# Optimization experiments

Hardware: AMD Instinct MI355X
Metric: run time of the kernel (lower is better)

Reference implementation:

```python
import jax, jax.numpy as jnp
import numpy as np

N = 20000      # nodes
E = 320000     # edges (before self-loops)
F_IN = 50      # PPI num_features
C1 = 256       # per-head channels, conv1/conv2
H1 = 4         # heads, conv1/conv2
C3 = 121       # PPI num_classes, conv3 per-head channels
H3 = 6         # heads, conv3 (concat=False -> mean)


def gat_conv(x, src, dst, W, a_src, a_dst, b, heads, ch, concat, n):
    """PyG-style GATConv with self-loops already included in (src, dst).
    Messages flow src -> dst; softmax is over incoming edges of each dst node."""
    h = (x @ W).reshape(n, heads, ch)                      # [N, H, C]
    es = jnp.sum(h * a_src, axis=-1)                       # [N, H]
    ed = jnp.sum(h * a_dst, axis=-1)                       # [N, H]
    e = jax.nn.leaky_relu(es[src] + ed[dst], 0.2)          # [E', H]
    m = jax.ops.segment_max(e, dst, num_segments=n)        # stable softmax per dst
    e = jnp.exp(e - m[dst])
    denom = jax.ops.segment_sum(e, dst, num_segments=n)
    alpha = e / jnp.maximum(denom[dst], 1e-16)             # [E', H]
    out = jax.ops.segment_sum(alpha[:, :, None] * h[src], dst, num_segments=n)  # [N, H, C]
    out = out.reshape(n, heads * ch) if concat else out.mean(axis=1)
    return out + b


def setup_inputs() -> dict:
    key = jax.random.key(0)
    ks = jax.random.split(key, 16)

    def p(k, shape, fan_in):
        return (jax.random.normal(k, shape, jnp.float32) / np.float32(np.sqrt(fan_in)))

    x = jax.random.normal(ks[0], (N, F_IN), jnp.float32)
    edge_index = jax.random.randint(ks[1], (2, E), 0, N, dtype=jnp.int64)
    D1 = H1 * C1  # 1024
    return dict(
        x=x, edge_index=edge_index,
        W1=p(ks[2], (F_IN, D1), F_IN), a1s=p(ks[3], (H1, C1), C1), a1d=p(ks[4], (H1, C1), C1), b1=jnp.zeros((D1,), jnp.float32),
        Wl1=p(ks[5], (F_IN, D1), F_IN), bl1=jnp.zeros((D1,), jnp.float32),
        W2=p(ks[6], (D1, D1), D1), a2s=p(ks[7], (H1, C1), C1), a2d=p(ks[8], (H1, C1), C1), b2=jnp.zeros((D1,), jnp.float32),
        Wl2=p(ks[9], (D1, D1), D1), bl2=jnp.zeros((D1,), jnp.float32),
        W3=p(ks[10], (D1, H3 * C3), D1), a3s=p(ks[11], (H3, C3), C3), a3d=p(ks[12], (H3, C3), C3), b3=jnp.zeros((C3,), jnp.float32),
        Wl3=p(ks[13], (D1, C3), D1), bl3=jnp.zeros((C3,), jnp.float32),
    )


def reference(x, edge_index, W1, a1s, a1d, b1, Wl1, bl1, W2, a2s, a2d, b2, Wl2, bl2, W3, a3s, a3d, b3, Wl3, bl3):
    n = x.shape[0]
    loop = jnp.arange(n, dtype=edge_index.dtype)           # PyG GATConv adds self-loops
    src = jnp.concatenate([edge_index[0], loop])
    dst = jnp.concatenate([edge_index[1], loop])
    x1 = jax.nn.elu(gat_conv(x, src, dst, W1, a1s, a1d, b1, H1, C1, True, n) + x @ Wl1 + bl1)
    x2 = jax.nn.elu(gat_conv(x1, src, dst, W2, a2s, a2d, b2, H1, C1, True, n) + x1 @ Wl2 + bl2)
    out = gat_conv(x2, src, dst, W3, a3s, a3d, b3, H3, C3, False, n) + x2 @ Wl3 + bl3
    return out
```

## Files before the change

kernel.cpp:

```cpp
#include <hip/hip_runtime.h>
#include <hip/hip_bf16.h>
#include <math.h>

typedef __bf16 bf16;
typedef __attribute__((ext_vector_type(4))) __bf16 bf16x4;
typedef __attribute__((ext_vector_type(8))) __bf16 bf16x8;
typedef __attribute__((ext_vector_type(4))) float f32x4;

#define N_NODES 20000
#define N_EDGES 320000
#define E2 (N_EDGES + N_NODES)
#define F_IN 50
#define D1 1024
#define NP12 2048
#define NP3 896
#define SG 2048
#define KA 320

#define PO_A1S 0
#define PO_A1D 1024
#define PO_B1  2048
#define PO_BL1 3072
#define PO_A2S 4096
#define PO_A2D 5120
#define PO_B2  6144
#define PO_BL2 7168
#define PO_A3S 8192
#define PO_A3D 8918
#define PO_B3  9644
#define PO_BL3 9765
#define PO_END 9886

__device__ __forceinline__ int clampi(int v, int lo, int hi)
{
    return v < lo ? lo : (v > hi ? hi : v);
}

__device__ __forceinline__ float loadf(const void* p, long idx, int isb)
{
    return isb ? (float)((const bf16*)p)[idx] : ((const float*)p)[idx];
}

__device__ __forceinline__ int loadei(const int* ei, long idx, int i64)
{
    return i64 ? ei[2 * idx] : ei[idx];
}

__global__ void k_detect(const int* __restrict__ ei,
                         const unsigned short* __restrict__ xw,
                         int* __restrict__ flags)
{
    if (blockIdx.x != 0 || threadIdx.x != 0) return;
    int allz = 1;
    for (int i = 0; i < 128; ++i)
        if (ei[2 * i + 1] != 0) { allz = 0; break; }
    int inr = 0;
    for (int i = 0; i < 128; ++i) {
        int e = (xw[2 * i] >> 7) & 0xFF;
        if (e >= 100 && e <= 140) inr++;
    }
    flags[0] = allz;
    flags[1] = (inr >= 64) ? 1 : 0;
}

template <bool BACT>
__global__ __launch_bounds__(256) void k_gemm(const bf16* __restrict__ A,
                                              const bf16* __restrict__ Bt,
                                              bf16* __restrict__ C,
                                              int M, int K, int lda, int ldb, int ldc,
                                              int mtiles, int ntiles,
                                              const bf16* __restrict__ bias)
{
    __shared__ bf16 As[128 * 64];
    __shared__ bf16 Bs[128 * 64];

    int id = blockIdx.x;
    int gfull = mtiles >> 3;
    int base  = gfull * 8 * ntiles;
    int x, y;
    if (id < base) {
        int gsz = 8 * ntiles;
        int g = id / gsz;
        int r = id - g * gsz;
        x = g * 8 + (r & 7);
        y = r >> 3;
    } else {
        int rem = mtiles - (gfull << 3);
        int r = id - base;
        x = (gfull << 3) + r % rem;
        y = r / rem;
    }
    const int m0 = x * 128;
    const int n0 = y * 128;

    const int tid  = threadIdx.x;
    const int wave = tid >> 6;
    const int lane = tid & 63;
    const int wm   = (wave >> 1) * 64;
    const int wn   = (wave & 1) * 64;
    const int frow  = lane & 15;

    const int srow = wave * 32 + (lane >> 3);
    const int scol = (((lane & 7) ^ (lane >> 3)) * 8);

    f32x4 acc[4][4];
#pragma unroll
    for (int i = 0; i < 4; ++i)
#pragma unroll
        for (int j = 0; j < 4; ++j)
#pragma unroll
            for (int r = 0; r < 4; ++r) acc[i][j][r] = 0.f;

    for (int k0 = 0; k0 < K; k0 += 64) {
#pragma unroll
        for (int i = 0; i < 4; ++i) {
            int ra = srow + i * 8;
            int ga = m0 + ra; if (ga > M - 1) ga = M - 1;
            __builtin_amdgcn_global_load_lds(
                (const __attribute__((address_space(1))) void*)(A + (size_t)ga * lda + k0 + scol),
                (__attribute__((address_space(3))) void*)(As + wave * 2048 + i * 512),
                16, 0, 0);
            int gb = n0 + ra;
            __builtin_amdgcn_global_load_lds(
                (const __attribute__((address_space(1))) void*)(Bt + (size_t)gb * ldb + k0 + scol),
                (__attribute__((address_space(3))) void*)(Bs + wave * 2048 + i * 512),
                16, 0, 0);
        }
        __syncthreads();
#pragma unroll
        for (int kk = 0; kk < 2; ++kk) {
            const int coff = (((kk * 4 + (lane >> 4)) ^ (frow & 7)) << 3);
            bf16x8 af[4], bfr[4];
#pragma unroll
            for (int i = 0; i < 4; ++i) {
                af[i]  = *(const bf16x8*)(As + (wm + i * 16 + frow) * 64 + coff);
                bfr[i] = *(const bf16x8*)(Bs + (wn + i * 16 + frow) * 64 + coff);
            }
#pragma unroll
            for (int i = 0; i < 4; ++i)
#pragma unroll
                for (int j = 0; j < 4; ++j)
                    acc[i][j] = __builtin_amdgcn_mfma_f32_16x16x32_bf16(af[i], bfr[j], acc[i][j], 0, 0, 0);
        }
        __syncthreads();
    }

#pragma unroll
    for (int i = 0; i < 4; ++i) {
#pragma unroll
        for (int j = 0; j < 4; ++j) {
            int rbase = m0 + wm + i * 16 + (lane >> 4) * 4;
            int col   = n0 + wn + j * 16 + frow;
            if constexpr (BACT) {
                float bv = (float)bias[col];
#pragma unroll
                for (int r = 0; r < 4; ++r) {
                    int row = rbase + r;
                    if (row < M) {
                        float v = acc[i][j][r] + bv;
                        v = (v > 0.f) ? v : (__expf(v) - 1.f);
                        C[(size_t)row * ldc + col] = (bf16)v;
                    }
                }
            } else {
#pragma unroll
                for (int r = 0; r < 4; ++r) {
                    int row = rbase + r;
                    if (row < M) C[(size_t)row * ldc + col] = (bf16)acc[i][j][r];
                }
            }
        }
    }
}

__global__ void k_padx(const void* __restrict__ x, bf16* __restrict__ A2,
                       const int* __restrict__ flags)
{
    int idx = blockIdx.x * 256 + threadIdx.x;
    if (idx >= N_NODES * 64) return;
    int isb = flags[1];
    int n = idx >> 6, k = idx & 63;
    A2[(size_t)n * KA + 256 + k] = (k < F_IN) ? (bf16)loadf(x, (long)n * F_IN + k, isb)
                                              : (bf16)0.f;
}

__global__ __launch_bounds__(256) void k_veca(const void* __restrict__ W1,
                                              const void* __restrict__ a1s,
                                              const void* __restrict__ a1d,
                                              const void* __restrict__ b1,
                                              const void* __restrict__ bl1,
                                              float* __restrict__ ws, float* __restrict__ wd,
                                              bf16* __restrict__ bsum,
                                              const int* __restrict__ flags)
{
    const int isb = flags[1];
    const int k = blockIdx.x;
    const int h = threadIdx.x >> 6;
    const int c0 = threadIdx.x & 63;
    float s = 0.f, d = 0.f;
    if (k < F_IN) {
        for (int c = c0; c < 256; c += 64) {
            float wv = loadf(W1, (long)k * D1 + h * 256 + c, isb);
            s += wv * loadf(a1s, h * 256 + c, isb);
            d += wv * loadf(a1d, h * 256 + c, isb);
        }
    }
#pragma unroll
    for (int off = 32; off; off >>= 1) {
        s += __shfl_xor(s, off);
        d += __shfl_xor(d, off);
    }
    if (c0 == 0) { ws[k * 4 + h] = s; wd[k * 4 + h] = d; }
    if (k < 4) {
        int j = k * 256 + threadIdx.x;
        bsum[j] = (bf16)(loadf(b1, j, isb) + loadf(bl1, j, isb));
    }
}

__global__ void k_wfuse1(const void* __restrict__ W1, const void* __restrict__ Wl1,
                         bf16* __restrict__ Bt, const int* __restrict__ flags)
{
    int idx = blockIdx.x * 256 + threadIdx.x;
    if (idx >= D1 * KA) return;
    int isb = flags[1];
    int j = idx / KA;
    int kp = idx - j * KA;
    float v = 0.f;
    if (kp < 256) {
        int hp = kp >> 6, k = kp & 63;
        if ((j >> 8) == hp && k < F_IN) v = loadf(W1, (long)k * D1 + j, isb);
    } else {
        int k = kp - 256;
        if (k < F_IN) v = loadf(Wl1, (long)k * D1 + j, isb);
    }
    Bt[idx] = (bf16)v;
}

__global__ __launch_bounds__(256) void k_wcatT(const void* __restrict__ Wa,
                                               const void* __restrict__ Wb,
                                               bf16* __restrict__ Bt,
                                               int split, int da, int db,
                                               const int* __restrict__ flags)
{
    __shared__ bf16 T[64][65];
    const int isb = flags[1];
    const int k0 = blockIdx.x * 64;
    const int n0 = blockIdx.y * 64;
    const int r = threadIdx.x >> 6;
    const int c = threadIdx.x & 63;
    const int n = n0 + c;
#pragma unroll
    for (int kk = 0; kk < 16; ++kk) {
        int k = k0 + r + kk * 4;
        float v = 0.f;
        if (n < split)           v = loadf(Wa, (long)k * da + n, isb);
        else if (n < split + db) v = loadf(Wb, (long)k * db + (n - split), isb);
        T[r + kk * 4][c] = (bf16)v;
    }
    __syncthreads();
#pragma unroll
    for (int kk = 0; kk < 16; ++kk) {
        int nn = r + kk * 4;
        Bt[(size_t)(n0 + nn) * 1024 + k0 + c] = T[c][nn];
    }
}

struct P12 { const void* s[12]; };

__global__ void k_params(P12 ps, bf16* __restrict__ pool, const int* __restrict__ flags)
{
    const int off[13] = {PO_A1S, PO_A1D, PO_B1, PO_BL1, PO_A2S, PO_A2D, PO_B2,
                         PO_BL2, PO_A3S, PO_A3D, PO_B3, PO_BL3, PO_END};
    int idx = blockIdx.x * 256 + threadIdx.x;
    if (idx >= PO_END) return;
    int isb = flags[1];
    int seg = 0;
    while (idx >= off[seg + 1]) seg++;
    pool[idx] = (bf16)loadf(ps.s[seg], idx - off[seg], isb);
}

__global__ void k_count(const int* __restrict__ ei, int* __restrict__ cnt,
                        const int* __restrict__ flags)
{
    int e = blockIdx.x * 256 + threadIdx.x;
    if (e >= E2) return;
    int i64 = flags[0];
    int d = (e < N_EDGES) ? loadei(ei, (long)N_EDGES + e, i64) : (e - N_EDGES);
    d = clampi(d, 0, N_NODES - 1);
    atomicAdd(&cnt[d], 1);
}

__global__ __launch_bounds__(256) void k_scan(const int* __restrict__ cnt, int* __restrict__ rp)
{
    __shared__ int ssum[256];
    int tid = threadIdx.x;
    const int chunk = (N_NODES + 255) / 256;
    int lo = tid * chunk;
    int hi = lo + chunk; if (hi > N_NODES) hi = N_NODES;
    int s = 0;
    for (int i = lo; i < hi; ++i) s += cnt[i];
    ssum[tid] = s;
    __syncthreads();
    if (tid == 0) {
        int run = 0;
        for (int i = 0; i < 256; ++i) { int t = ssum[i]; ssum[i] = run; run += t; }
        rp[N_NODES] = run;
    }
    __syncthreads();
    int run = ssum[tid];
    for (int i = lo; i < hi; ++i) { rp[i] = run; run += cnt[i]; }
}

__global__ void k_copy(const int* __restrict__ rp, int* __restrict__ cur)
{
    int i = blockIdx.x * 256 + threadIdx.x;
    if (i < N_NODES) cur[i] = rp[i];
}

__global__ void k_fill(const int* __restrict__ ei, int* __restrict__ cur,
                       int* __restrict__ ss, const int* __restrict__ flags)
{
    int e = blockIdx.x * 256 + threadIdx.x;
    if (e >= E2) return;
    int i64 = flags[0];
    int s, d;
    if (e < N_EDGES) {
        s = loadei(ei, e, i64);
        d = loadei(ei, (long)N_EDGES + e, i64);
    } else {
        s = e - N_EDGES; d = s;
    }
    s = clampi(s, 0, N_NODES - 1);
    d = clampi(d, 0, N_NODES - 1);
    int pos = atomicAdd(&cur[d], 1);
    if (pos >= 0 && pos < E2) ss[pos] = s;
}

__global__ __launch_bounds__(256) void k_logits1(const bf16* __restrict__ A2,
                                                 const float* __restrict__ ws,
                                                 const float* __restrict__ wd,
                                                 float* __restrict__ es, float* __restrict__ ed)
{
    const int wave = threadIdx.x >> 6;
    const int lane = threadIdx.x & 63;
    const int n = blockIdx.x * 4 + wave;
    if (n >= N_NODES) return;
    float xv = (float)A2[(size_t)n * KA + 256 + lane];
    f32x4 wsv = *(const f32x4*)(ws + lane * 4);
    f32x4 wdv = *(const f32x4*)(wd + lane * 4);
    float s[4], d[4];
#pragma unroll
    for (int h = 0; h < 4; ++h) { s[h] = xv * wsv[h]; d[h] = xv * wdv[h]; }
#pragma unroll
    for (int off = 32; off; off >>= 1)
#pragma unroll
        for (int h = 0; h < 4; ++h) {
            s[h] += __shfl_xor(s[h], off);
            d[h] += __shfl_xor(d[h], off);
        }
    if (lane == 0) {
#pragma unroll
        for (int h = 0; h < 4; ++h) { es[n * 4 + h] = s[h]; ed[n * 4 + h] = d[h]; }
    }
}

__global__ __launch_bounds__(256) void k_aggx(bf16* __restrict__ A2,
                                              const float* __restrict__ es,
                                              const float* __restrict__ ed,
                                              const int* __restrict__ rp,
                                              const int* __restrict__ ss)
{
    __shared__ float smx[4], sinv[4], sed[4];
    __shared__ float sal[64 * 4];
    __shared__ int   ssrc[64];

    const int n   = blockIdx.x;
    const int tid = threadIdx.x;
    int r0 = clampi(rp[n], 0, E2);
    int r1 = clampi(rp[n + 1], r0, E2);
    const int deg = r1 - r0;

    const int sw = tid >> 5, ln = tid & 31;
    if (sw < 4) {
        int h = sw;
        float edn = ed[n * 4 + h];
        float mx = -1e30f;
        for (int e = ln; e < deg; e += 32) {
            int s = clampi(ss[r0 + e], 0, N_NODES - 1);
            float w = es[s * 4 + h] + edn;
            w = (w > 0.f) ? w : 0.2f * w;
            mx = fmaxf(mx, w);
        }
#pragma unroll
        for (int off = 16; off; off >>= 1) mx = fmaxf(mx, __shfl_xor(mx, off, 32));
        float sm = 0.f;
        for (int e = ln; e < deg; e += 32) {
            int s = clampi(ss[r0 + e], 0, N_NODES - 1);
            float w = es[s * 4 + h] + edn;
            w = (w > 0.f) ? w : 0.2f * w;
            sm += __expf(w - mx);
        }
#pragma unroll
        for (int off = 16; off; off >>= 1) sm += __shfl_xor(sm, off, 32);
        if (ln == 0) { smx[h] = mx; sinv[h] = 1.f / fmaxf(sm, 1e-16f); sed[h] = edn; }
    }
    __syncthreads();

    const int k  = tid & 63;
    const int hh = tid >> 6;
    float acc = 0.f;

    for (int e0 = 0; e0 < deg; e0 += 64) {
        int ce = min(64, deg - e0);
        int ce4 = (ce + 3) & ~3;
        __syncthreads();
        if (tid < ce4 * 4) {
            int e = tid >> 2, h = tid & 3;
            int valid = (e < ce);
            int s = valid ? clampi(ss[r0 + e0 + e], 0, N_NODES - 1) : 0;
            float w = es[s * 4 + h] + sed[h];
            w = (w > 0.f) ? w : 0.2f * w;
            sal[e * 4 + h] = valid ? __expf(w - smx[h]) * sinv[h] : 0.f;
            if (h == 0) ssrc[e] = s;
        }
        __syncthreads();
        for (int e = 0; e < ce4; e += 4) {
            float xv[4], al[4];
#pragma unroll
            for (int p = 0; p < 4; ++p) {
                int s = ssrc[e + p];
                xv[p] = (float)A2[(size_t)s * KA + 256 + k];
            }
#pragma unroll
            for (int p = 0; p < 4; ++p) al[p] = sal[(e + p) * 4 + hh];
#pragma unroll
            for (int p = 0; p < 4; ++p) acc += al[p] * xv[p];
        }
    }
    A2[(size_t)n * KA + hh * 64 + k] = (bf16)acc;
}

template <int H, int C>
__global__ __launch_bounds__(256) void k_logits(const bf16* __restrict__ G,
                                                const bf16* __restrict__ as_,
                                                const bf16* __restrict__ ad_,
                                                float* __restrict__ es, float* __restrict__ ed)
{
    const int wave = threadIdx.x >> 6;
    const int lane = threadIdx.x & 63;
    const int n = blockIdx.x * 4 + wave;
    if (n >= N_NODES) return;

#pragma unroll
    for (int h = 0; h < H; ++h) {
        float s = 0.f, d = 0.f;
        if constexpr (C == 256) {
            bf16x4 g  = *(const bf16x4*)(G + (size_t)n * SG + h * 256 + lane * 4);
            bf16x4 av = *(const bf16x4*)(as_ + h * 256 + lane * 4);
            bf16x4 dv = *(const bf16x4*)(ad_ + h * 256 + lane * 4);
#pragma unroll
            for (int j = 0; j < 4; ++j) {
                float gv = (float)g[j];
                s += gv * (float)av[j];
                d += gv * (float)dv[j];
            }
        } else {
            for (int c = lane; c < C; c += 64) {
                float hv = (float)G[(size_t)n * SG + h * C + c];
                s += hv * (float)as_[h * C + c];
                d += hv * (float)ad_[h * C + c];
            }
        }
#pragma unroll
        for (int off = 32; off; off >>= 1) {
            s += __shfl_xor(s, off);
            d += __shfl_xor(d, off);
        }
        if (lane == 0) { es[n * H + h] = s; ed[n * H + h] = d; }
    }
}

template <int H, int C, bool MEAN, bool ELU, bool EXTOUT>
__global__ __launch_bounds__(256) void k_agg(const bf16* __restrict__ G,
                                             const bf16* __restrict__ S,
                                             const float* __restrict__ es,
                                             const float* __restrict__ ed,
                                             const int* __restrict__ rp,
                                             const int* __restrict__ ss,
                                             const bf16* __restrict__ bgat,
                                             const bf16* __restrict__ bskip,
                                             void* __restrict__ out, int sout,
                                             const int* __restrict__ flags)
{
    constexpr int D  = H * C;
    constexpr int NV = (D + 3) / 4;
    constexpr int CH = 256;
    __shared__ float smx[H], sinv[H], sed[H];
    __shared__ float sal[CH * H];
    __shared__ int   ssrc[CH];

    const int n   = blockIdx.x;
    const int tid = threadIdx.x;
    int r0 = clampi(rp[n], 0, E2);
    int r1 = clampi(rp[n + 1], r0, E2);
    const int deg = r1 - r0;

    const int sw = tid >> 5, ln = tid & 31;
    for (int h = sw; h < H; h += 8) {
        float edn = ed[n * H + h];
        float mx = -1e30f;
        for (int e = ln; e < deg; e += 32) {
            int s = clampi(ss[r0 + e], 0, N_NODES - 1);
            float w = es[s * H + h] + edn;
            w = (w > 0.f) ? w : 0.2f * w;
            mx = fmaxf(mx, w);
        }
#pragma unroll
        for (int off = 16; off; off >>= 1) mx = fmaxf(mx, __shfl_xor(mx, off, 32));
        float sm = 0.f;
        for (int e = ln; e < deg; e += 32) {
            int s = clampi(ss[r0 + e], 0, N_NODES - 1);
            float w = es[s * H + h] + edn;
            w = (w > 0.f) ? w : 0.2f * w;
            sm += __expf(w - mx);
        }
#pragma unroll
        for (int off = 16; off; off >>= 1) sm += __shfl_xor(sm, off, 32);
        if (ln == 0) { smx[h] = mx; sinv[h] = 1.f / fmaxf(sm, 1e-16f); sed[h] = edn; }
    }
    __syncthreads();

    const int c0 = tid * 4;
    const int hA = (c0 < D) ? (c0 / C) : 0;
    const int hB = (c0 + 3 < D) ? ((c0 + 3) / C) : hA;
    int hj1 = ((c0 + 1 < D) ? ((c0 + 1) / C) : hA) == hA;
    int hj2 = ((c0 + 2 < D) ? ((c0 + 2) / C) : hA) == hA;
    const bool active = (tid < NV);

    float acc[4] = {0.f, 0.f, 0.f, 0.f};

    for (int e0 = 0; e0 < deg; e0 += CH) {
        int ce = min(CH, deg - e0);
        int ce4 = (ce + 3) & ~3;
        __syncthreads();
        for (int t = tid; t < ce4 * H; t += 256) {
            int e = t / H, h = t - e * H;
            int valid = (e < ce);
            int s = valid ? clampi(ss[r0 + e0 + e], 0, N_NODES - 1) : 0;
            float w = es[s * H + h] + sed[h];
            w = (w > 0.f) ? w : 0.2f * w;
            sal[e * H + h] = valid ? __expf(w - smx[h]) * sinv[h] : 0.f;
            if (h == 0) ssrc[e] = s;
        }
        __syncthreads();
        if (active) {
            for (int eb = 0; eb < ce4; eb += 4) {
                int sg[4];
#pragma unroll
                for (int p = 0; p < 4; ++p) sg[p] = ssrc[eb + p];
                bf16x4 g[4];
#pragma unroll
                for (int p = 0; p < 4; ++p)
                    g[p] = *(const bf16x4*)(G + (size_t)sg[p] * SG + c0);
                if constexpr (C % 4 == 0) {
                    float a[4];
#pragma unroll
                    for (int p = 0; p < 4; ++p) a[p] = sal[(eb + p) * H + hA];
#pragma unroll
                    for (int p = 0; p < 4; ++p)
#pragma unroll
                        for (int j = 0; j < 4; ++j)
                            acc[j] += a[p] * (float)g[p][j];
                } else {
#pragma unroll
                    for (int p = 0; p < 4; ++p) {
                        float aL = sal[(eb + p) * H + hA];
                        float aH = sal[(eb + p) * H + hB];
                        acc[0] += aL * (float)g[p][0];
                        acc[1] += (hj1 ? aL : aH) * (float)g[p][1];
                        acc[2] += (hj2 ? aL : aH) * (float)g[p][2];
                        acc[3] += aH * (float)g[p][3];
                    }
                }
            }
        }
    }

    const int outbf = EXTOUT ? flags[1] : 1;

    if constexpr (!MEAN) {
        if (active) {
            bf16x4 bg = *(const bf16x4*)(bgat + c0);
            bf16x4 sk = *(const bf16x4*)(S + (size_t)n * SG + c0);
            bf16x4 bs = *(const bf16x4*)(bskip + c0);
            bf16x4 ov;
#pragma unroll
            for (int j = 0; j < 4; ++j) {
                float v = acc[j] + (float)bg[j] + (float)sk[j] + (float)bs[j];
                if (ELU) v = (v > 0.f) ? v : (__expf(v) - 1.f);
                ov[j] = (bf16)v;
            }
            *(bf16x4*)((bf16*)out + (size_t)n * sout + c0) = ov;
        }
    } else {
        __shared__ float sagg[D];
        if (active) {
#pragma unroll
            for (int j = 0; j < 4; ++j) {
                int c = c0 + j;
                if (c < D) sagg[c] = acc[j];
            }
        }
        __syncthreads();
        for (int c = tid; c < C; c += 256) {
            float v = 0.f;
#pragma unroll
            for (int h = 0; h < H; ++h) v += sagg[h * C + c];
            v *= (1.f / H);
            v += (float)bgat[c] + (float)S[(size_t)n * SG + c] + (float)bskip[c];
            if (outbf) ((bf16*)out)[(size_t)n * sout + c] = (bf16)v;
            else       ((float*)out)[(size_t)n * sout + c] = v;
        }
    }
}

extern "C" void kernel_launch(void* const* d_in, const int* in_sizes, int n_in,
                              void* d_out, int out_size, void* d_ws, size_t ws_size,
                              hipStream_t stream)
{
    const void* x   = d_in[0];
    const int*  ei  = (const int*)d_in[1];
    const void* W1  = d_in[2];
    const void* Wl1 = d_in[6];
    const void* W2  = d_in[8];
    const void* Wl2 = d_in[12];
    const void* W3  = d_in[14];
    const void* Wl3 = d_in[18];

    P12 ps;
    ps.s[0] = d_in[3];  ps.s[1] = d_in[4];  ps.s[2] = d_in[5];  ps.s[3] = d_in[7];
    ps.s[4] = d_in[9];  ps.s[5] = d_in[10]; ps.s[6] = d_in[11]; ps.s[7] = d_in[13];
    ps.s[8] = d_in[15]; ps.s[9] = d_in[16]; ps.s[10] = d_in[17]; ps.s[11] = d_in[19];

    char* w = (char*)d_ws;
    auto alloc = [&](size_t bytes) {
        char* p = w;
        w += (bytes + 255) & ~(size_t)255;
        return p;
    };
    int*   flags = (int*)alloc(64);
    int*   cnt   = (int*)alloc((size_t)N_NODES * 4);
    int*   rp    = (int*)alloc((size_t)(N_NODES + 1) * 4);
    int*   cur   = (int*)alloc((size_t)N_NODES * 4);
    int*   ss    = (int*)alloc((size_t)E2 * 4);
    float* es    = (float*)alloc((size_t)N_NODES * 6 * 4);
    float* ed    = (float*)alloc((size_t)N_NODES * 6 * 4);
    bf16*  pool  = (bf16*)alloc((size_t)PO_END * 2);
    float* ws1   = (float*)alloc((size_t)64 * 4 * 4);
    float* wd1   = (float*)alloc((size_t)64 * 4 * 4);
    bf16*  bsum  = (bf16*)alloc((size_t)D1 * 2);
    bf16*  Bt    = (bf16*)alloc((size_t)NP12 * 1024 * 2);
    bf16*  X     = (bf16*)alloc((size_t)N_NODES * D1 * 2);
    bf16*  WS    = (bf16*)alloc((size_t)N_NODES * SG * 2);
    bf16*  A2    = WS;

    k_detect<<<1, 64, 0, stream>>>(ei, (const unsigned short*)x, flags);

    hipMemsetAsync(cnt, 0, N_NODES * 4, stream);
    k_count<<<(E2 + 255) / 256, 256, 0, stream>>>(ei, cnt, flags);
    k_scan<<<1, 256, 0, stream>>>(cnt, rp);
    k_copy<<<(N_NODES + 255) / 256, 256, 0, stream>>>(rp, cur);
    k_fill<<<(E2 + 255) / 256, 256, 0, stream>>>(ei, cur, ss, flags);

    k_params<<<(PO_END + 255) / 256, 256, 0, stream>>>(ps, pool, flags);

    const dim3 blk(256);
    const int MT = (N_NODES + 127) / 128;

    k_veca<<<64, 256, 0, stream>>>(W1, ps.s[0], ps.s[1], ps.s[2], ps.s[3],
                                   ws1, wd1, bsum, flags);
    k_padx<<<(N_NODES * 64 + 255) / 256, 256, 0, stream>>>(x, A2, flags);
    k_wfuse1<<<(D1 * KA + 255) / 256, 256, 0, stream>>>(W1, Wl1, Bt, flags);
    k_logits1<<<N_NODES / 4, 256, 0, stream>>>(A2, ws1, wd1, es, ed);
    k_aggx<<<N_NODES, 256, 0, stream>>>(A2, es, ed, rp, ss);
    k_gemm<true><<<MT * (D1 / 128), blk, 0, stream>>>(A2, Bt, X, N_NODES, KA, KA, KA, D1,
                                                      MT, D1 / 128, bsum);

    k_wcatT<<<dim3(16, NP12 / 64), blk, 0, stream>>>(W2, Wl2, Bt, 1024, 1024, 1024, flags);
    k_gemm<false><<<MT * (NP12 / 128), blk, 0, stream>>>(X, Bt, WS, N_NODES, 1024, 1024, 1024, SG,
                                                         MT, NP12 / 128, nullptr);
    k_logits<4, 256><<<N_NODES / 4, 256, 0, stream>>>(WS, pool + PO_A2S, pool + PO_A2D, es, ed);
    k_agg<4, 256, false, true, false><<<N_NODES, 256, 0, stream>>>(
        WS, WS + D1, es, ed, rp, ss, pool + PO_B2, pool + PO_BL2, X, D1, flags);

    k_wcatT<<<dim3(16, NP3 / 64), blk, 0, stream>>>(W3, Wl3, Bt, 726, 726, 121, flags);
    k_gemm<false><<<MT * (NP3 / 128), blk, 0, stream>>>(X, Bt, WS, N_NODES, 1024, 1024, 1024, SG,
                                                        MT, NP3 / 128, nullptr);
    k_logits<6, 121><<<N_NODES / 4, 256, 0, stream>>>(WS, pool + PO_A3S, pool + PO_A3D, es, ed);
    k_agg<6, 121, true, false, true><<<N_NODES, 256, 0, stream>>>(
        WS, WS + 726, es, ed, rp, ss, pool + PO_B3, pool + PO_BL3, d_out, 121, flags);
}
```

Before: 645.6 us.

## Add 256x256-tile 8-wave GEMM with LDS direct loads for layers 2 and 3

```diff
diff --git a/kernel.cpp b/kernel.cpp
--- a/kernel.cpp
+++ b/kernel.cpp
@@ -13,7 +13,7 @@
 #define F_IN 50
 #define D1 1024
 #define NP12 2048
-#define NP3 896
+#define NP3 1024
 #define SG 2048
 #define KA 320
 
@@ -168,6 +168,153 @@
                     int row = rbase + r;
                     if (row < M) C[(size_t)row * ldc + col] = (bf16)acc[i][j][r];
                 }
+            }
+        }
+    }
+}
+
+__global__ __launch_bounds__(512, 2) void k_gemm256(const bf16* __restrict__ A,
+                                                    const bf16* __restrict__ Bt,
+                                                    bf16* __restrict__ C,
+                                                    int M, int K, int lda, int ldb, int ldc,
+                                                    int mtiles, int ntiles)
+{
+    __shared__ bf16 As[2][256 * 64];
+    __shared__ bf16 Bs[2][256 * 64];
+
+    int id = blockIdx.x;
+    int gfull = mtiles >> 3;
+    int base  = gfull * 8 * ntiles;
+    int x, y;
+    if (id < base) {
+        int gsz = 8 * ntiles;
+        int g = id / gsz;
+        int r = id - g * gsz;
+        x = g * 8 + (r & 7);
+        y = r >> 3;
+    } else {
+        int rem = mtiles - (gfull << 3);
+        int r = id - base;
+        x = (gfull << 3) + r % rem;
+        y = r / rem;
+    }
+    const int m0 = x * 256;
+    const int n0 = y * 256;
+
+    const int tid  = threadIdx.x;
+    const int wave = tid >> 6;
+    const int lane = tid & 63;
+    const int wr   = wave >> 2;
+    const int wc   = wave & 3;
+    const int frow = lane & 15;
+    const int hi   = lane >> 4;
+    const int sr8  = lane >> 3;
+    const int scol = (((lane & 7) ^ sr8) << 3);
+
+    auto stage_a = [&](int b, int h, int t1) {
+        const int k0s = t1 << 6;
+#pragma unroll
+        for (int i_ = 0; i_ < 2; ++i_) {
+            int row_ = h * 128 + i_ * 64 + wave * 8 + sr8;
+            int ga_ = m0 + row_; if (ga_ > M - 1) ga_ = M - 1;
+            __builtin_amdgcn_global_load_lds(
+                (const __attribute__((address_space(1))) void*)(A + (size_t)ga_ * lda + k0s + scol),
+                (__attribute__((address_space(3))) void*)(&As[b][(h * 128 + i_ * 64 + wave * 8) * 64]),
+                16, 0, 0);
+        }
+    };
+    auto stage_b = [&](int b, int h, int t1) {
+        const int k0s = t1 << 6;
+#pragma unroll
+        for (int i_ = 0; i_ < 2; ++i_) {
+            int row_ = h * 128 + i_ * 64 + wave * 8 + sr8;
+            int gb_ = n0 + row_;
+            __builtin_amdgcn_global_load_lds(
+                (const __attribute__((address_space(1))) void*)(Bt + (size_t)gb_ * ldb + k0s + scol),
+                (__attribute__((address_space(3))) void*)(&Bs[b][(h * 128 + i_ * 64 + wave * 8) * 64]),
+                16, 0, 0);
+        }
+    };
+
+    f32x4 acc[8][4];
+#pragma unroll
+    for (int i = 0; i < 8; ++i)
+#pragma unroll
+        for (int j = 0; j < 4; ++j)
+#pragma unroll
+            for (int r = 0; r < 4; ++r) acc[i][j][r] = 0.f;
+
+    auto compute = [&](int b, int MH, int NH) {
+        bf16x8 af[4][2], bv[2][2];
+#pragma unroll
+        for (int m_ = 0; m_ < 4; ++m_)
+#pragma unroll
+            for (int kk_ = 0; kk_ < 2; ++kk_)
+                af[m_][kk_] = *(const bf16x8*)&As[b][
+                    (wr * 128 + MH * 64 + m_ * 16 + frow) * 64 +
+                    (((kk_ * 4 + hi) ^ (frow & 7)) << 3)];
+#pragma unroll
+        for (int n_ = 0; n_ < 2; ++n_)
+#pragma unroll
+            for (int kk_ = 0; kk_ < 2; ++kk_)
+                bv[n_][kk_] = *(const bf16x8*)&Bs[b][
+                    (wc * 64 + NH * 32 + n_ * 16 + frow) * 64 +
+                    (((kk_ * 4 + hi) ^ (frow & 7)) << 3)];
+        __builtin_amdgcn_s_setprio(1);
+#pragma unroll
+        for (int kk_ = 0; kk_ < 2; ++kk_)
+#pragma unroll
+            for (int m_ = 0; m_ < 4; ++m_)
+#pragma unroll
+                for (int n_ = 0; n_ < 2; ++n_)
+                    acc[MH * 4 + m_][NH * 2 + n_] =
+                        __builtin_amdgcn_mfma_f32_16x16x32_bf16(
+                            af[m_][kk_], bv[n_][kk_],
+                            acc[MH * 4 + m_][NH * 2 + n_], 0, 0, 0);
+        __builtin_amdgcn_s_setprio(0);
+    };
+
+    stage_a(0, 0, 0);
+    stage_b(0, 0, 0);
+    stage_b(0, 1, 0);
+    stage_a(0, 1, 0);
+
+    const int nt = K >> 6;
+    int p = 0;
+#pragma unroll 1
+    for (int t = 0; t < nt - 1; ++t, p ^= 1) {
+        stage_a(p ^ 1, 0, t + 1);
+        asm volatile("s_waitcnt vmcnt(2)" ::: "memory");
+        __builtin_amdgcn_s_barrier();
+        compute(p, 0, 0);
+        __builtin_amdgcn_s_barrier();
+        stage_b(p ^ 1, 0, t + 1);
+        compute(p, 0, 1);
+        __builtin_amdgcn_s_barrier();
+        stage_b(p ^ 1, 1, t + 1);
+        compute(p, 1, 1);
+        __builtin_amdgcn_s_barrier();
+        stage_a(p ^ 1, 1, t + 1);
+        compute(p, 1, 0);
+        __builtin_amdgcn_s_barrier();
+    }
+    asm volatile("s_waitcnt vmcnt(0)" ::: "memory");
+    __builtin_amdgcn_s_barrier();
+    compute(p, 0, 0);
+    compute(p, 0, 1);
+    compute(p, 1, 1);
+    compute(p, 1, 0);
+
+#pragma unroll
+    for (int mf = 0; mf < 8; ++mf) {
+#pragma unroll
+        for (int nf = 0; nf < 4; ++nf) {
+            int row0 = m0 + wr * 128 + mf * 16 + hi * 4;
+            int col  = n0 + wc * 64 + nf * 16 + frow;
+#pragma unroll
+            for (int r = 0; r < 4; ++r) {
+                int row = row0 + r;
+                if (row < M) C[(size_t)row * ldc + col] = (bf16)acc[mf][nf][r];
             }
         }
     }
@@ -675,7 +822,8 @@
     k_params<<<(PO_END + 255) / 256, 256, 0, stream>>>(ps, pool, flags);
 
     const dim3 blk(256);
-    const int MT = (N_NODES + 127) / 128;
+    const int MT  = (N_NODES + 127) / 128;
+    const int MT2 = (N_NODES + 255) / 256;
 
     k_veca<<<64, 256, 0, stream>>>(W1, ps.s[0], ps.s[1], ps.s[2], ps.s[3],
                                    ws1, wd1, bsum, flags);
@@ -687,15 +835,15 @@
                                                       MT, D1 / 128, bsum);
 
     k_wcatT<<<dim3(16, NP12 / 64), blk, 0, stream>>>(W2, Wl2, Bt, 1024, 1024, 1024, flags);
-    k_gemm<false><<<MT * (NP12 / 128), blk, 0, stream>>>(X, Bt, WS, N_NODES, 1024, 1024, 1024, SG,
-                                                         MT, NP12 / 128, nullptr);
+    k_gemm256<<<MT2 * (NP12 / 256), 512, 0, stream>>>(X, Bt, WS, N_NODES, 1024, 1024, 1024, SG,
+                                                      MT2, NP12 / 256);
     k_logits<4, 256><<<N_NODES / 4, 256, 0, stream>>>(WS, pool + PO_A2S, pool + PO_A2D, es, ed);
     k_agg<4, 256, false, true, false><<<N_NODES, 256, 0, stream>>>(
         WS, WS + D1, es, ed, rp, ss, pool + PO_B2, pool + PO_BL2, X, D1, flags);
 
     k_wcatT<<<dim3(16, NP3 / 64), blk, 0, stream>>>(W3, Wl3, Bt, 726, 726, 121, flags);
-    k_gemm<false><<<MT * (NP3 / 128), blk, 0, stream>>>(X, Bt, WS, N_NODES, 1024, 1024, 1024, SG,
-                                                        MT, NP3 / 128, nullptr);
+    k_gemm256<<<MT2 * (NP3 / 256), 512, 0, stream>>>(X, Bt, WS, N_NODES, 1024, 1024, 1024, SG,
+                                                     MT2, NP3 / 256);
     k_logits<6, 121><<<N_NODES / 4, 256, 0, stream>>>(WS, pool + PO_A3S, pool + PO_A3D, es, ed);
     k_agg<6, 121, true, false, true><<<N_NODES, 256, 0, stream>>>(
         WS, WS + 726, es, ed, rp, ss, pool + PO_B3, pool + PO_BL3, d_out, 121, flags);
```

New measurement: 733.0 us. 1.14x slower.
